# Performance work log

Measured on AMD Instinct MI355X. Metric: run time of the kernel, lower is better.

Reference implementation:

```python
import jax, jax.numpy as jnp
import numpy as np

B, S, D, H = 4, 2048, 1024, 16
DK = D // H


def setup_inputs() -> dict:
    key = jax.random.key(0)
    ks = jax.random.split(key, 8)
    scale = 1.0 / np.sqrt(D)
    return {
        "q": jax.random.normal(ks[0], (B, S, D), jnp.float32),
        "k": jax.random.normal(ks[1], (B, S, D), jnp.float32),
        "v": jax.random.normal(ks[2], (B, S, D), jnp.float32),
        "mask": jnp.ones((1,), jnp.int32),  # unused (original code never applies it)
        "W_Q": jax.random.normal(ks[3], (D, D), jnp.float32) * scale,
        "W_K": jax.random.normal(ks[4], (D, D), jnp.float32) * scale,
        "W_V": jax.random.normal(ks[5], (D, D), jnp.float32) * scale,
        "W_O": jax.random.normal(ks[6], (D, D), jnp.float32) * scale,
    }


def reference(q, k, v, mask, W_Q, W_K, W_V, W_O):
    # nn.Linear(bias=False): y = x @ W.T ; weight shape [out, in]
    query = q @ W_Q.T  # [B,S,D]
    key_ = k @ W_K.T
    value = v @ W_V.T
    # split heads -> [B,H,S,DK]
    query = query.reshape(B, S, H, DK).transpose(0, 2, 1, 3)
    key_ = key_.reshape(B, S, H, DK).transpose(0, 2, 1, 3)
    value = value.reshape(B, S, H, DK).transpose(0, 2, 1, 3)
    # naive attention: full [B,H,S,S] score matrix (faithful to source)
    scores = jnp.einsum("bhqd,bhkd->bhqk", query, key_) / jnp.sqrt(
        jnp.asarray(DK, query.dtype)
    )
    attn = jax.nn.softmax(scores, axis=-1)  # dropout p=0.0 -> identity
    x = jnp.einsum("bhqk,bhkd->bhqd", attn, value)  # [B,H,S,DK]
    x = x.transpose(0, 2, 1, 3).reshape(B, S, D)
    return x @ W_O.T
```

## Files before the change

### kernel.cpp

```cpp
#include <hip/hip_runtime.h>
#include <math.h>


#define DEV __device__ __forceinline__

typedef __bf16 bf16x8 __attribute__((ext_vector_type(8)));
typedef __bf16 bf16x2 __attribute__((ext_vector_type(2)));
typedef float f32x4 __attribute__((ext_vector_type(4)));
typedef unsigned int u32x2 __attribute__((ext_vector_type(2)));

typedef __attribute__((address_space(1))) const unsigned int g_u32;
typedef __attribute__((address_space(3))) unsigned int l_u32;

DEV unsigned short f2bf(float x) {
  unsigned int u = __float_as_uint(x);
  u += 0x7fffu + ((u >> 16) & 1u);
  return (unsigned short)(u >> 16);
}

DEV unsigned int pack2bf(float a, float b) {
#if __has_builtin(__builtin_amdgcn_cvt_pk_bf16_f32)
  bf16x2 r = __builtin_amdgcn_cvt_pk_bf16_f32(a, b);
  union { bf16x2 v; unsigned int u; } c;
  c.v = r;
  return c.u;
#else
  unsigned int ua = __float_as_uint(a) + 0x8000u;
  unsigned int ub = __float_as_uint(b) + 0x8000u;
  return (ua >> 16) | (ub & 0xffff0000u);
#endif
}

DEV float fexp2(float x) {
#if __has_builtin(__builtin_amdgcn_exp2f)
  return __builtin_amdgcn_exp2f(x);
#else
  return __expf(x * 0.69314718056f);
#endif
}

DEV void ld16(const unsigned short* g, unsigned short* l) {
  __builtin_amdgcn_global_load_lds((g_u32*)g, (l_u32*)l, 16, 0, 0);
}

__global__ __launch_bounds__(256) void cast_all(
    const float* __restrict__ q, const float* __restrict__ k,
    const float* __restrict__ v, const float* __restrict__ w0,
    const float* __restrict__ w1, const float* __restrict__ w2,
    const float* __restrict__ w3, unsigned short* __restrict__ qb,
    unsigned short* __restrict__ kb, unsigned short* __restrict__ vb,
    unsigned short* __restrict__ o0, unsigned short* __restrict__ o1,
    unsigned short* __restrict__ o2, unsigned short* __restrict__ o3) {
  const int bb = blockIdx.x;
  const float* src;
  unsigned short* dst;
  int i;
  if (bb < 24576) {
    const int z = bb >> 13, lb = bb & 8191;
    src = (z == 0) ? q : (z == 1) ? k : v;
    dst = (z == 0) ? qb : (z == 1) ? kb : vb;
    i = lb * 256 + threadIdx.x;
  } else {
    const int t = bb - 24576;
    const int z = t >> 10, lb = t & 1023;
    src = (z == 0) ? w0 : (z == 1) ? w1 : (z == 2) ? w2 : w3;
    dst = (z == 0) ? o0 : (z == 1) ? o1 : (z == 2) ? o2 : o3;
    i = lb * 256 + threadIdx.x;
  }
  float4 vv = reinterpret_cast<const float4*>(src)[i];
  ushort4 o;
  o.x = f2bf(vv.x); o.y = f2bf(vv.y); o.z = f2bf(vv.z); o.w = f2bf(vv.w);
  reinterpret_cast<ushort4*>(dst)[i] = o;
}

template <bool SW>
DEV void gemm_core(const unsigned short* __restrict__ A,
                   const unsigned short* __restrict__ W,
                   unsigned short* As, unsigned short* Bs,
                   f32x4 (&acc)[4][4], int tileM, int tileN) {
  const int tid = threadIdx.x;
  const int w = tid >> 6, lane = tid & 63;
  const int wr = (w & 1) * 64, wc = (w >> 1) * 64;
  const int l15 = lane & 15, g4 = lane >> 4, l7 = l15 & 7;
  const int rsub = lane >> 3;
  const int gsrc = (lane & 7) ^ rsub;

  const f32x4 fzero = {0.f, 0.f, 0.f, 0.f};
#pragma unroll
  for (int i = 0; i < 4; i++)
#pragma unroll
    for (int j = 0; j < 4; j++) acc[i][j] = fzero;

  for (int k0 = 0; k0 < 1024; k0 += 64) {
#pragma unroll
    for (int j = 0; j < 4; ++j) {
      const int c = w * 4 + j;
      ld16(A + (size_t)(tileM + c * 8 + rsub) * 1024 + k0 + gsrc * 8, As + c * 512);
      ld16(W + (size_t)(tileN + c * 8 + rsub) * 1024 + k0 + gsrc * 8, Bs + c * 512);
    }
    __syncthreads();
#pragma unroll
    for (int kc = 0; kc < 2; kc++) {
      const int ph = ((kc * 4 + g4) ^ l7) * 8;
      bf16x8 aF[4], bF[4];
#pragma unroll
      for (int i = 0; i < 4; i++)
        aF[i] = *reinterpret_cast<const bf16x8*>(&As[(wr + i * 16 + l15) * 64 + ph]);
#pragma unroll
      for (int j = 0; j < 4; j++)
        bF[j] = *reinterpret_cast<const bf16x8*>(&Bs[(wc + j * 16 + l15) * 64 + ph]);
#pragma unroll
      for (int i = 0; i < 4; i++)
#pragma unroll
        for (int j = 0; j < 4; j++) {
          if (SW)
            acc[j][i] = __builtin_amdgcn_mfma_f32_16x16x32_bf16(bF[j], aF[i], acc[j][i], 0, 0, 0);
          else
            acc[i][j] = __builtin_amdgcn_mfma_f32_16x16x32_bf16(aF[i], bF[j], acc[i][j], 0, 0, 0);
        }
    }
    __syncthreads();
  }
}

__global__ __launch_bounds__(256) void gemm_qkv(
    const unsigned short* __restrict__ qb, const unsigned short* __restrict__ kb,
    const unsigned short* __restrict__ vb, const unsigned short* __restrict__ Wq,
    const unsigned short* __restrict__ Wk, const unsigned short* __restrict__ Wv,
    unsigned short* __restrict__ Qp, unsigned short* __restrict__ Kp,
    unsigned short* __restrict__ VpT) {
  __shared__ __align__(16) unsigned short As[128 * 64];
  __shared__ __align__(16) unsigned short Bs[128 * 64];
  const int z = blockIdx.z;
  const int tileM = blockIdx.x * 128, tileN = blockIdx.y * 128;
  const int tid = threadIdx.x, w = tid >> 6, lane = tid & 63;
  const int wr = (w & 1) * 64, wc = (w >> 1) * 64;
  const int l15 = lane & 15, g4 = lane >> 4;
  f32x4 acc[4][4];

  if (z < 2) {
    gemm_core<true>((z == 0) ? qb : kb, (z == 0) ? Wq : Wk, As, Bs, acc, tileM, tileN);
    const float qs = (z == 0) ? 0.125f * 1.44269504089f : 1.0f;
    unsigned short* C = (z == 0) ? Qp : Kp;
#pragma unroll
    for (int i = 0; i < 4; i++) {
      const size_t row = (size_t)(tileM + wr + i * 16 + l15);
#pragma unroll
      for (int j = 0; j < 4; j++) {
        const int col = tileN + wc + j * 16 + g4 * 4;
        ushort4 pk;
        pk.x = f2bf(acc[j][i][0] * qs); pk.y = f2bf(acc[j][i][1] * qs);
        pk.z = f2bf(acc[j][i][2] * qs); pk.w = f2bf(acc[j][i][3] * qs);
        *reinterpret_cast<ushort4*>(&C[row * 1024 + col]) = pk;
      }
    }
  } else {
    gemm_core<false>(vb, Wv, As, Bs, acc, tileM, tileN);
    const int b = tileM / 2048, s0 = tileM % 2048;
#pragma unroll
    for (int i = 0; i < 4; i++)
#pragma unroll
      for (int j = 0; j < 4; j++) {
        int col = tileN + wc + j * 16 + l15;
        int s = s0 + wr + i * 16 + g4 * 4;
        ushort4 pk;
        pk.x = f2bf(acc[i][j][0]); pk.y = f2bf(acc[i][j][1]);
        pk.z = f2bf(acc[i][j][2]); pk.w = f2bf(acc[i][j][3]);
        *reinterpret_cast<ushort4*>(&VpT[(size_t)(b * 1024 + col) * 2048 + s]) = pk;
      }
  }
}

__global__ __launch_bounds__(256) void gemm_out(
    const unsigned short* __restrict__ Xp, const unsigned short* __restrict__ Wo,
    float* __restrict__ out) {
  __shared__ __align__(16) unsigned short As[128 * 64];
  __shared__ __align__(16) unsigned short Bs[128 * 64];
  const int tileM = blockIdx.x * 128, tileN = blockIdx.y * 128;
  f32x4 acc[4][4];
  gemm_core<true>(Xp, Wo, As, Bs, acc, tileM, tileN);
  const int tid = threadIdx.x, w = tid >> 6, lane = tid & 63;
  const int wr = (w & 1) * 64, wc = (w >> 1) * 64;
  const int l15 = lane & 15, g4 = lane >> 4;
#pragma unroll
  for (int i = 0; i < 4; i++) {
    const size_t row = (size_t)(tileM + wr + i * 16 + l15);
#pragma unroll
    for (int j = 0; j < 4; j++) {
      const int col = tileN + wc + j * 16 + g4 * 4;
      *reinterpret_cast<f32x4*>(&out[row * 1024 + col]) = acc[j][i];
    }
  }
}

__global__ __launch_bounds__(256, 4) void attn(
    const unsigned short* __restrict__ Qp, const unsigned short* __restrict__ Kp,
    const unsigned short* __restrict__ VpT, unsigned short* __restrict__ Xp) {
  __shared__ __align__(16) unsigned short Ks[64 * 64];
  __shared__ __align__(16) unsigned short Vs[64 * 64];
  __shared__ __align__(16) unsigned short Ps[4 * 16 * 64];

  const int bid = blockIdx.x;
  const int nid = (bid & 7) * 128 + (bid >> 3);
  const int qt = nid & 15, bh = nid >> 4;
  const int b = bh >> 4, h = bh & 15;
  const int q0 = qt * 128;
  const int tid = threadIdx.x, w = tid >> 6, lane = tid & 63;
  const int l15 = lane & 15, g4 = lane >> 4;
  const int l7 = l15 & 7;

  const int rsub = lane >> 3;
  const int gsrc = (lane & 7) ^ rsub;

  bf16x8 qf[2][2];
#pragma unroll
  for (int mi = 0; mi < 2; mi++) {
    const unsigned short* Qrow =
        Qp + (size_t)(b * 2048 + q0 + w * 32 + mi * 16 + l15) * 1024 + h * 64;
    qf[mi][0] = *reinterpret_cast<const bf16x8*>(Qrow + g4 * 8);
    qf[mi][1] = *reinterpret_cast<const bf16x8*>(Qrow + 32 + g4 * 8);
  }

  const f32x4 fzero = {0.f, 0.f, 0.f, 0.f};
  f32x4 o[2][4];
#pragma unroll
  for (int mi = 0; mi < 2; mi++)
#pragma unroll
    for (int dj = 0; dj < 4; dj++) o[mi][dj] = fzero;
  float l_i[2] = {0.f, 0.f};

  const unsigned short* Kbase = Kp + (size_t)(b * 2048) * 1024 + h * 64;
  const unsigned short* Vbase = VpT + (size_t)(b * 1024 + h * 64) * 2048;
  unsigned short* Pw = Ps + w * 1024;

  for (int kt = 0; kt < 2048; kt += 64) {
#pragma unroll
    for (int j = 0; j < 2; ++j) {
      const int c = w * 2 + j;
      ld16(Kbase + (size_t)(kt + c * 8 + rsub) * 1024 + gsrc * 8, Ks + c * 512);
      ld16(Vbase + (size_t)(c * 8 + rsub) * 2048 + kt + gsrc * 8, Vs + c * 512);
    }
    __syncthreads();

    f32x4 sv[2][4];
    __builtin_amdgcn_s_setprio(1);
#pragma unroll
    for (int jt = 0; jt < 4; jt++) {
      const int row = jt * 16 + l15;
      const int s0 = g4 ^ l7;
      bf16x8 kf0 = *reinterpret_cast<const bf16x8*>(&Ks[row * 64 + s0 * 8]);
      bf16x8 kf1 = *reinterpret_cast<const bf16x8*>(&Ks[row * 64 + (s0 ^ 4) * 8]);
#pragma unroll
      for (int mi = 0; mi < 2; mi++) {
        f32x4 z = fzero;
        z = __builtin_amdgcn_mfma_f32_16x16x32_bf16(kf0, qf[mi][0], z, 0, 0, 0);
        z = __builtin_amdgcn_mfma_f32_16x16x32_bf16(kf1, qf[mi][1], z, 0, 0, 0);
        sv[mi][jt] = z;
      }
    }
    __builtin_amdgcn_s_setprio(0);

#pragma unroll
    for (int mi = 0; mi < 2; mi++) {
      float rs = 0.f;
#pragma unroll
      for (int jt = 0; jt < 4; jt++)
#pragma unroll
        for (int r = 0; r < 4; r++) {
          sv[mi][jt][r] = fexp2(sv[mi][jt][r]);
          rs += sv[mi][jt][r];
        }
      l_i[mi] += rs;
    }

    bf16x8 vf[2][4];
#pragma unroll
    for (int kc = 0; kc < 2; kc++)
#pragma unroll
      for (int dj = 0; dj < 4; dj++)
        vf[kc][dj] = *reinterpret_cast<const bf16x8*>(
            &Vs[(dj * 16 + l15) * 64 + ((kc * 4 + g4) ^ l7) * 8]);

#pragma unroll
    for (int mi = 0; mi < 2; mi++) {
#pragma unroll
      for (int jt = 0; jt < 4; jt++) {
        u32x2 pk;
        pk.x = pack2bf(sv[mi][jt][0], sv[mi][jt][1]);
        pk.y = pack2bf(sv[mi][jt][2], sv[mi][jt][3]);
        const int slot = (jt * 4 + g4) ^ l15;
        *reinterpret_cast<u32x2*>(&Pw[l15 * 64 + slot * 4]) = pk;
      }
      __builtin_amdgcn_s_setprio(1);
#pragma unroll
      for (int kc = 0; kc < 2; kc++) {
        const int sA = (kc * 8 + g4 * 2) ^ l15;
        const int sB = (kc * 8 + g4 * 2 + 1) ^ l15;
        u32x2 pa = *reinterpret_cast<const u32x2*>(&Pw[l15 * 64 + sA * 4]);
        u32x2 pb = *reinterpret_cast<const u32x2*>(&Pw[l15 * 64 + sB * 4]);
        union { unsigned int u[4]; bf16x8 v; } pf;
        pf.u[0] = pa.x; pf.u[1] = pa.y; pf.u[2] = pb.x; pf.u[3] = pb.y;
#pragma unroll
        for (int dj = 0; dj < 4; dj++)
          o[mi][dj] = __builtin_amdgcn_mfma_f32_16x16x32_bf16(vf[kc][dj], pf.v,
                                                             o[mi][dj], 0, 0, 0);
      }
      __builtin_amdgcn_s_setprio(0);
    }
    __syncthreads();
  }

#pragma unroll
  for (int mi = 0; mi < 2; mi++) {
    float rs = l_i[mi];
    rs += __shfl_xor(rs, 16);
    rs += __shfl_xor(rs, 32);
    const float inv = 1.f / rs;
    const size_t row = (size_t)(b * 2048 + q0 + w * 32 + mi * 16 + l15);
#pragma unroll
    for (int dj = 0; dj < 4; dj++) {
      ushort4 pk;
      pk.x = f2bf(o[mi][dj][0] * inv);
      pk.y = f2bf(o[mi][dj][1] * inv);
      pk.z = f2bf(o[mi][dj][2] * inv);
      pk.w = f2bf(o[mi][dj][3] * inv);
      *reinterpret_cast<ushort4*>(&Xp[row * 1024 + h * 64 + dj * 16 + g4 * 4]) = pk;
    }
  }
}

extern "C" void kernel_launch(void* const* d_in, const int* in_sizes, int n_in,
                              void* d_out, int out_size, void* d_ws, size_t ws_size,
                              hipStream_t stream) {
  const float* q  = (const float*)d_in[0];
  const float* k  = (const float*)d_in[1];
  const float* v  = (const float*)d_in[2];
  const float* Wq = (const float*)d_in[4];
  const float* Wk = (const float*)d_in[5];
  const float* Wv = (const float*)d_in[6];
  const float* Wo = (const float*)d_in[7];
  float* out = (float*)d_out;

  char* ws = (char*)d_ws;
  const size_t MB = 1u << 20;
  unsigned short* qb  = (unsigned short*)(ws + 0 * MB);
  unsigned short* kb  = (unsigned short*)(ws + 16 * MB);
  unsigned short* vb  = (unsigned short*)(ws + 32 * MB);
  unsigned short* wqb = (unsigned short*)(ws + 48 * MB);
  unsigned short* wkb = (unsigned short*)(ws + 50 * MB);
  unsigned short* wvb = (unsigned short*)(ws + 52 * MB);
  unsigned short* wob = (unsigned short*)(ws + 54 * MB);
  unsigned short* Qp  = (unsigned short*)(ws + 56 * MB);
  unsigned short* Kp  = (unsigned short*)(ws + 72 * MB);
  unsigned short* VpT = (unsigned short*)(ws + 88 * MB);
  unsigned short* Xp  = (unsigned short*)(ws + 104 * MB);

  cast_all<<<dim3(28672), 256, 0, stream>>>(q, k, v, Wq, Wk, Wv, Wo,
                                            qb, kb, vb, wqb, wkb, wvb, wob);

  dim3 gq(64, 8, 3);
  gemm_qkv<<<gq, 256, 0, stream>>>(qb, kb, vb, wqb, wkb, wvb, Qp, Kp, VpT);

  attn<<<dim3(1024), 256, 0, stream>>>(Qp, Kp, VpT, Xp);

  dim3 go(64, 8, 1);
  gemm_out<<<go, 256, 0, stream>>>(Xp, wob, out);
}
```

Baseline: 359.0 us.

## Double-buffer K/V tiles in attention to overlap loads with compute

Adds a second LDS buffer for the K and V tiles, prefetches the next tile while the current one is being computed, and drops one barrier per iteration. The aim is to hide global-to-LDS load latency behind the MFMA and softmax work. LDS use rises from about 24KB to 40KB per block, which may lower occupancy below the 4 blocks per CU requested by the launch bounds. Correctness depends on ld16 completing before the single end-of-iteration barrier, and it is unclear whether ld16 is an async direct-to-LDS load that needs a vmcnt wait.

```diff
diff --git a/kernel.cpp b/kernel.cpp
--- a/kernel.cpp
+++ b/kernel.cpp
@@ -196,8 +196,8 @@
 __global__ __launch_bounds__(256, 4) void attn(
     const unsigned short* __restrict__ Qp, const unsigned short* __restrict__ Kp,
     const unsigned short* __restrict__ VpT, unsigned short* __restrict__ Xp) {
-  __shared__ __align__(16) unsigned short Ks[64 * 64];
-  __shared__ __align__(16) unsigned short Vs[64 * 64];
+  __shared__ __align__(16) unsigned short Ks[2 * 64 * 64];
+  __shared__ __align__(16) unsigned short Vs[2 * 64 * 64];
   __shared__ __align__(16) unsigned short Ps[4 * 16 * 64];
 
   const int bid = blockIdx.x;
@@ -233,14 +233,33 @@
   const unsigned short* Vbase = VpT + (size_t)(b * 1024 + h * 64) * 2048;
   unsigned short* Pw = Ps + w * 1024;
 
-  for (int kt = 0; kt < 2048; kt += 64) {
-#pragma unroll
-    for (int j = 0; j < 2; ++j) {
-      const int c = w * 2 + j;
-      ld16(Kbase + (size_t)(kt + c * 8 + rsub) * 1024 + gsrc * 8, Ks + c * 512);
-      ld16(Vbase + (size_t)(c * 8 + rsub) * 2048 + kt + gsrc * 8, Vs + c * 512);
-    }
-    __syncthreads();
+  const int c = w * 2;
+
+#pragma unroll
+  for (int j = 0; j < 2; ++j) {
+    ld16(Kbase + (size_t)((c + j) * 8 + rsub) * 1024 + gsrc * 8, Ks + (c + j) * 512);
+    ld16(Vbase + (size_t)((c + j) * 8 + rsub) * 2048 + gsrc * 8, Vs + (c + j) * 512);
+  }
+  __syncthreads();
+
+  int cur = 0;
+  for (int t = 0; t < 32; ++t) {
+    const int kt = t * 64;
+    unsigned short* Kc = Ks + cur * 4096;
+    unsigned short* Vc = Vs + cur * 4096;
+
+    if (t < 31) {
+      unsigned short* Kn = Ks + (cur ^ 1) * 4096;
+      unsigned short* Vn = Vs + (cur ^ 1) * 4096;
+      const int ktn = kt + 64;
+#pragma unroll
+      for (int j = 0; j < 2; ++j) {
+        ld16(Kbase + (size_t)(ktn + (c + j) * 8 + rsub) * 1024 + gsrc * 8,
+             Kn + (c + j) * 512);
+        ld16(Vbase + (size_t)((c + j) * 8 + rsub) * 2048 + ktn + gsrc * 8,
+             Vn + (c + j) * 512);
+      }
+    }
 
     f32x4 sv[2][4];
     __builtin_amdgcn_s_setprio(1);
@@ -248,8 +267,8 @@
     for (int jt = 0; jt < 4; jt++) {
       const int row = jt * 16 + l15;
       const int s0 = g4 ^ l7;
-      bf16x8 kf0 = *reinterpret_cast<const bf16x8*>(&Ks[row * 64 + s0 * 8]);
-      bf16x8 kf1 = *reinterpret_cast<const bf16x8*>(&Ks[row * 64 + (s0 ^ 4) * 8]);
+      bf16x8 kf0 = *reinterpret_cast<const bf16x8*>(&Kc[row * 64 + s0 * 8]);
+      bf16x8 kf1 = *reinterpret_cast<const bf16x8*>(&Kc[row * 64 + (s0 ^ 4) * 8]);
 #pragma unroll
       for (int mi = 0; mi < 2; mi++) {
         f32x4 z = fzero;
@@ -279,7 +298,7 @@
 #pragma unroll
       for (int dj = 0; dj < 4; dj++)
         vf[kc][dj] = *reinterpret_cast<const bf16x8*>(
-            &Vs[(dj * 16 + l15) * 64 + ((kc * 4 + g4) ^ l7) * 8]);
+            &Vc[(dj * 16 + l15) * 64 + ((kc * 4 + g4) ^ l7) * 8]);
 
 #pragma unroll
     for (int mi = 0; mi < 2; mi++) {
@@ -307,7 +326,9 @@
       }
       __builtin_amdgcn_s_setprio(0);
     }
+
     __syncthreads();
+    cur ^= 1;
   }
 
 #pragma unroll
```

Result: no change. 365.6 us (+1.8%).
